# Optimization experiments

Measured on AMD Instinct MI355X. Metric: run time of the kernel, lower is better.

The kernel has to match this reference:

```python
import jax, jax.numpy as jnp
import numpy as np

B, S, D, H = 2, 2048, 1024, 16
DH = D // H


def setup_inputs() -> dict:
    key = jax.random.key(0)
    ks = jax.random.split(key, 7)
    scale = 1.0 / np.sqrt(D)
    queries = jax.random.normal(ks[0], (B, S, D), dtype=jnp.float32)
    keys_ = jax.random.normal(ks[1], (B, S, D), dtype=jnp.float32)
    values = jax.random.normal(ks[2], (B, S, D), dtype=jnp.float32)
    mask = jnp.tril(jnp.ones((S, S), dtype=jnp.int32))[None, None]  # causal [1,1,S,S]
    Wq = jax.random.normal(ks[3], (D, D), dtype=jnp.float32) * scale
    Wk = jax.random.normal(ks[4], (D, D), dtype=jnp.float32) * scale
    Wv = jax.random.normal(ks[5], (D, D), dtype=jnp.float32) * scale
    Wo = jax.random.normal(ks[6], (D, D), dtype=jnp.float32) * scale
    return {"queries": queries, "keys": keys_, "values": values, "mask": mask,
            "Wq": Wq, "Wk": Wk, "Wv": Wv, "Wo": Wo}


def reference(queries, keys, values, mask, Wq, Wk, Wv, Wo):
    # linear projections (nn.Linear, no bias): x @ W.T
    def split_heads(x, W):
        return (x @ W.T).reshape(B, -1, H, DH).transpose(0, 2, 1, 3)  # [B,H,S,DH]

    q = split_heads(queries, Wq)
    k = split_heads(keys, Wk)
    v = split_heads(values, Wv)

    scores = jnp.einsum('bhqd,bhkd->bhqk', q, k) / jnp.sqrt(jnp.float32(DH))
    scores = jnp.where(mask == 0, jnp.float32(-jnp.inf), scores)
    weights = jax.nn.softmax(scores, axis=-1)  # dropout p=0.0 -> identity
    out = jnp.einsum('bhqk,bhkd->bhqd', weights, v)
    out = out.transpose(0, 2, 1, 3).reshape(B, -1, D)
    return out @ Wo.T
```

## Files before the change

kernel.cpp:

```cpp
#include <hip/hip_runtime.h>
#include <hip/hip_bf16.h>


typedef unsigned short u16;
typedef __attribute__((ext_vector_type(8))) short bf16x8;
typedef __attribute__((ext_vector_type(4))) float f32x4;
typedef __attribute__((ext_vector_type(4))) short s16x4;

#define DEVI static __device__ __forceinline__
#define SCL 0.18033688011112042f
#define GLDS(g, l) __builtin_amdgcn_global_load_lds( \
    (const __attribute__((address_space(1))) unsigned*)(g), \
    (__attribute__((address_space(3))) unsigned*)(l), 16, 0, 0)

DEVI u16 f2bf(float f) {
  __hip_bfloat16 h = __float2bfloat16(f);
  union { __hip_bfloat16 h; u16 u; } c; c.h = h;
  return c.u;
}

DEVI bf16x8 cvt8(f32x4 a, f32x4 b) {
  bf16x8 r;
  r[0] = (short)f2bf(a[0]); r[1] = (short)f2bf(a[1]);
  r[2] = (short)f2bf(a[2]); r[3] = (short)f2bf(a[3]);
  r[4] = (short)f2bf(b[0]); r[5] = (short)f2bf(b[1]);
  r[6] = (short)f2bf(b[2]); r[7] = (short)f2bf(b[3]);
  return r;
}

template <int F32>
DEVI void load_pair(f32x4* lo, f32x4* hi, bf16x8* bb, const void* P,
                    size_t o0, size_t o1) {
  if constexpr (F32) {
    const float* p0 = (const float*)P + o0;
    const float* p1 = (const float*)P + o1;
    lo[0] = *(const f32x4*)p0; hi[0] = *(const f32x4*)(p0 + 4);
    lo[1] = *(const f32x4*)p1; hi[1] = *(const f32x4*)(p1 + 4);
  } else {
    bb[0] = *(const bf16x8*)((const u16*)P + o0);
    bb[1] = *(const bf16x8*)((const u16*)P + o1);
  }
}

template <int F32>
DEVI void finish_pair(f32x4* lo, f32x4* hi, bf16x8* bb, u16* dst, int e0, int e1) {
  if constexpr (F32) { bb[0] = cvt8(lo[0], hi[0]); bb[1] = cvt8(lo[1], hi[1]); }
  *(bf16x8*)(dst + e0) = bb[0];
  *(bf16x8*)(dst + e1) = bb[1];
}

template <int MODE, int O32>
DEVI void epilogue(f32x4 (&acc)[4][4], void* C, int tileM, int tileN,
                   int wr, int wc, int lr, int lg, float oscale) {
  constexpr int N = 1024;
  if constexpr (MODE == 0) {
#pragma unroll
    for (int m = 0; m < 4; ++m) {
      const int row0 = tileM + wr + m * 16 + lg * 4;
#pragma unroll
      for (int n = 0; n < 4; ++n) {
        const int col = tileN + wc + n * 16 + lr;
#pragma unroll
        for (int j = 0; j < 4; ++j) {
          if constexpr (O32)
            ((float*)C)[(size_t)(row0 + j) * N + col] = acc[m][n][j] * oscale;
          else
            ((u16*)C)[(size_t)(row0 + j) * N + col] = f2bf(acc[m][n][j] * oscale);
        }
      }
    }
  } else if constexpr (MODE == 1) {
    u16* Cv = (u16*)C;
#pragma unroll
    for (int m = 0; m < 4; ++m) {
      const int row0 = tileM + wr + m * 16 + lg * 4;
      const int bb = row0 >> 11, s0 = row0 & 2047;
#pragma unroll
      for (int n = 0; n < 4; ++n) {
        const int col = tileN + wc + n * 16 + lr;
        s16x4 pk;
#pragma unroll
        for (int j = 0; j < 4; ++j) pk[j] = (short)f2bf(acc[m][n][j]);
        *(s16x4*)(Cv + ((size_t)(col + (bb << 10)) << 11) + s0) = pk;
      }
    }
  } else {
    u16* Cv = (u16*)C;
#pragma unroll
    for (int m = 0; m < 4; ++m) {
      const int row0 = tileM + wr + m * 16 + lg * 4;
      const int bb = row0 >> 11, s0 = row0 & 2047;
#pragma unroll
      for (int n = 0; n < 4; ++n) {
        const int col = tileN + wc + n * 16 + lr;
        const size_t base = ((size_t)((bb << 4) + (col >> 6)) * 2048 + s0) * 64 + (col & 63);
#pragma unroll
        for (int j = 0; j < 4; ++j)
          Cv[base + (size_t)j * 64] = f2bf(acc[m][n][j]);
      }
    }
  }
}

template <int A32, int W32, int MODE, int O32>
DEVI void gemm_core(u16* sA0, u16* sA1, u16* sB0, u16* sB1,
                    const void* A, const void* W, void* C,
                    int tileM, int tileN, float oscale) {
  constexpr int K = 1024;
  const int tid = threadIdx.x;
  const int lane = tid & 63;
  const int wave = tid >> 6;
  const int wr = (wave >> 1) * 64;
  const int wc = (wave & 1) * 64;
  const int lr = lane & 15, lg = lane >> 4;

  f32x4 acc[4][4] = {};

  const int e0 = tid * 8;
  const int e1 = 2048 + tid * 8;
  const int r0 = e0 >> 5, c0 = e0 & 31;
  const int r1 = e1 >> 5, c1 = e1 & 31;
  const size_t oA0 = (size_t)(tileM + r0) * K + c0;
  const size_t oA1 = (size_t)(tileM + r1) * K + c1;
  const size_t oB0 = (size_t)(tileN + r0) * K + c0;
  const size_t oB1 = (size_t)(tileN + r1) * K + c1;

  f32x4 alo[2], ahi[2], blo[2], bhi[2];
  bf16x8 ab[2], bb[2];

  load_pair<A32>(alo, ahi, ab, A, oA0, oA1);
  load_pair<W32>(blo, bhi, bb, W, oB0, oB1);
  finish_pair<A32>(alo, ahi, ab, sA0, e0, e1);
  finish_pair<W32>(blo, bhi, bb, sB0, e0, e1);
  __syncthreads();

  for (int k0 = 0; k0 < K; k0 += 32) {
    u16* cA = (k0 & 32) ? sA1 : sA0;
    u16* cB = (k0 & 32) ? sB1 : sB0;
    u16* nA = (k0 & 32) ? sA0 : sA1;
    u16* nB = (k0 & 32) ? sB0 : sB1;

    bf16x8 af[4], bfr[4];
#pragma unroll
    for (int m = 0; m < 4; ++m)
      af[m] = *(const bf16x8*)(cA + (wr + m * 16 + lr) * 32 + lg * 8);
#pragma unroll
    for (int n = 0; n < 4; ++n)
      bfr[n] = *(const bf16x8*)(cB + (wc + n * 16 + lr) * 32 + lg * 8);

    const bool more = (k0 + 32 < K);
    if (more) {
      load_pair<A32>(alo, ahi, ab, A, oA0 + k0 + 32, oA1 + k0 + 32);
      load_pair<W32>(blo, bhi, bb, W, oB0 + k0 + 32, oB1 + k0 + 32);
    }

#pragma unroll
    for (int m = 0; m < 4; ++m)
#pragma unroll
      for (int n = 0; n < 4; ++n)
        acc[m][n] = __builtin_amdgcn_mfma_f32_16x16x32_bf16(af[m], bfr[n], acc[m][n], 0, 0, 0);

    if (more) {
      finish_pair<A32>(alo, ahi, ab, nA, e0, e1);
      finish_pair<W32>(blo, bhi, bb, nB, e0, e1);
    }
    __syncthreads();
  }
  epilogue<MODE, O32>(acc, C, tileM, tileN, wr, wc, lr, lg, oscale);
}

DEVI void tile_remap(int& tileM, int& tileN) {
  const int i = blockIdx.x + 8 * blockIdx.y;
  const int c = i & 7, s = i >> 3;
  tileM = (c * 4 + (s & 3)) * 128;
  tileN = (s >> 2) * 128;
}

template <int IN32>
__global__ void __launch_bounds__(256, 3)
gemm_qkv(const void* __restrict__ q, const void* __restrict__ wq, u16* __restrict__ Qp,
         const void* __restrict__ k, const void* __restrict__ wk, u16* __restrict__ Kh,
         const void* __restrict__ v, const void* __restrict__ wv, u16* __restrict__ Vt) {
  __shared__ __align__(16) u16 sA[2][128 * 32];
  __shared__ __align__(16) u16 sB[2][128 * 32];
  int tileM, tileN;
  tile_remap(tileM, tileN);
  if (blockIdx.z == 0)
    gemm_core<IN32, IN32, 0, 0>(sA[0], sA[1], sB[0], sB[1], q, wq, Qp, tileM, tileN, SCL);
  else if (blockIdx.z == 1)
    gemm_core<IN32, IN32, 2, 0>(sA[0], sA[1], sB[0], sB[1], k, wk, Kh, tileM, tileN, 1.f);
  else
    gemm_core<IN32, IN32, 1, 0>(sA[0], sA[1], sB[0], sB[1], v, wv, Vt, tileM, tileN, 1.f);
}

template <int W32, int O32>
__global__ void __launch_bounds__(256, 3)
gemm_out(const u16* __restrict__ A, const void* __restrict__ W, void* __restrict__ C) {
  __shared__ __align__(16) u16 sA[2][128 * 32];
  __shared__ __align__(16) u16 sB[2][128 * 32];
  int tileM, tileN;
  tile_remap(tileM, tileN);
  gemm_core<0, W32, 0, O32>(sA[0], sA[1], sB[0], sB[1], A, W, C, tileM, tileN, 1.f);
}


DEVI void stage_klds(const u16* __restrict__ Kb, const u16* __restrict__ Vb,
                     u16* sKb, u16* sVb, int kt, int w, int lane) {
  const int kr = lane >> 3;
  const int kg = (lane & 7) ^ kr;
  const u16* gk = Kb + (size_t)(kt + w * 16 + kr) * 64 + kg * 8;
  const int vr = lane >> 2;
  const int vg = (lane & 3) ^ ((lane >> 3) & 3);
  const u16* gv = Vb + (size_t)(w * 32 + vr) * 2048 + kt + vg * 8;
  u16* dk = sKb + w * 1024;
  u16* dv = sVb + w * 1024;
  GLDS(gk, dk);
  GLDS(gk + 8 * 64, dk + 512);
  GLDS(gv, dv);
  GLDS(gv + (size_t)16 * 2048, dv + 512);
}

__global__ void __launch_bounds__(128, 3)
attn_kernel(const u16* Qp, const u16* __restrict__ Kh,
            const u16* __restrict__ Vt, u16* AO) {
  __shared__ __align__(16) u16 sK[3][2048];
  __shared__ __align__(16) u16 sV[3][2048];
  const int tid = threadIdx.x;
  const int lane = tid & 63;
  const int w = tid >> 6;
  const int lr = lane & 15;
  const int lg = lane >> 4;

  const int id = blockIdx.x;
  const int xcd = id & 7;
  const int slot = id >> 3;
  const int bh = xcd * 4 + (slot & 3);
  const int band = 63 - (slot >> 2);
  const int b = bh >> 4;
  const int h = bh & 15;
  const int r0 = band * 32;

  const u16* Kb = Kh + (size_t)bh * 2048 * 64;
  const u16* Vb = Vt + (size_t)bh * 64 * 2048;

  const int qrow = r0 + w * 16 + lr;
  const u16* Qw = Qp + ((size_t)(b * 2048 + qrow) << 10) + h * 64;
  const bf16x8 qf0 = *(const bf16x8*)(Qw + lg * 8);
  const bf16x8 qf1 = *(const bf16x8*)(Qw + 32 + lg * 8);

  f32x4 o[4] = {};
  float mr = -INFINITY, ls = 0.f;
  const int nt = band + 1;

  stage_klds(Kb, Vb, sK[0], sV[0], 0, w, lane);

#pragma unroll 1
  for (int t = 0; t < nt; ++t) {
    if (t + 1 < nt) {
      const int bi = (t + 1) % 3;
      stage_klds(Kb, Vb, sK[bi], sV[bi], (t + 1) * 32, w, lane);
      asm volatile("s_waitcnt vmcnt(4)" ::: "memory");
    } else {
      asm volatile("s_waitcnt vmcnt(0)" ::: "memory");
    }
    asm volatile("s_barrier" ::: "memory");
    __builtin_amdgcn_s_setprio(1);

    {
      const int bi = t % 3;
      const u16* sKb = sK[bi];
      const u16* sVb = sV[bi];
      const int sw = lr & 7;
      const bf16x8 kf0 = *(const bf16x8*)(sKb + lr * 64 + ((lg ^ sw) * 8));
      const bf16x8 kf1 = *(const bf16x8*)(sKb + lr * 64 + (((4 + lg) ^ sw) * 8));
      const bf16x8 kf2 = *(const bf16x8*)(sKb + (16 + lr) * 64 + ((lg ^ sw) * 8));
      const bf16x8 kf3 = *(const bf16x8*)(sKb + (16 + lr) * 64 + (((4 + lg) ^ sw) * 8));

      const f32x4 z = {};
      f32x4 s0 = __builtin_amdgcn_mfma_f32_16x16x32_bf16(kf0, qf0, z, 0, 0, 0);
      s0 = __builtin_amdgcn_mfma_f32_16x16x32_bf16(kf1, qf1, s0, 0, 0, 0);
      f32x4 s1 = __builtin_amdgcn_mfma_f32_16x16x32_bf16(kf2, qf0, z, 0, 0, 0);
      s1 = __builtin_amdgcn_mfma_f32_16x16x32_bf16(kf3, qf1, s1, 0, 0, 0);

      float p[8];
#pragma unroll
      for (int j = 0; j < 4; ++j) { p[j] = s0[j]; p[4 + j] = s1[j]; }
      if (t == nt - 1) {
        const int kt0 = t * 32;
#pragma unroll
        for (int j = 0; j < 4; ++j) {
          if (kt0 + lg * 4 + j > qrow)      p[j] = -INFINITY;
          if (kt0 + 16 + lg * 4 + j > qrow) p[4 + j] = -INFINITY;
        }
      }

      const float tm = fmaxf(fmaxf(fmaxf(p[0], p[1]), fmaxf(p[2], p[3])),
                             fmaxf(fmaxf(p[4], p[5]), fmaxf(p[6], p[7])));
      if (!__all(tm <= mr + 11.5f)) {
        float tr_ = fmaxf(tm, __shfl_xor(tm, 16));
        tr_ = fmaxf(tr_, __shfl_xor(tr_, 32));
        const float mn = fmaxf(mr, tr_);
        const float fac = exp2f(mr - mn);
        mr = mn;
        ls *= fac;
#pragma unroll
        for (int j = 0; j < 4; ++j) {
          const float fj = __shfl(fac, lg * 4 + j);
#pragma unroll
          for (int d = 0; d < 4; ++d) o[d][j] *= fj;
        }
      }

#pragma unroll
      for (int i = 0; i < 8; ++i) p[i] = exp2f(p[i] - mr);
      ls += ((p[0] + p[1]) + (p[2] + p[3])) + ((p[4] + p[5]) + (p[6] + p[7]));

      bf16x8 pa;
#pragma unroll
      for (int i = 0; i < 8; ++i) pa[i] = (short)f2bf(p[i]);

      const int s2 = (lr >> 1) & 3;
#pragma unroll
      for (int d = 0; d < 4; ++d) {
        const u16* vrow = sVb + (16 * d + lr) * 32;
        const s16x4 v0 = *(const s16x4*)(vrow + (((lg >> 1) ^ s2) * 8) + (lg & 1) * 4);
        const s16x4 v1 = *(const s16x4*)(vrow + ((((lg >> 1) + 2) ^ s2) * 8) + (lg & 1) * 4);
        bf16x8 vf;
        vf[0] = v0[0]; vf[1] = v0[1]; vf[2] = v0[2]; vf[3] = v0[3];
        vf[4] = v1[0]; vf[5] = v1[1]; vf[6] = v1[2]; vf[7] = v1[3];
        o[d] = __builtin_amdgcn_mfma_f32_16x16x32_bf16(pa, vf, o[d], 0, 0, 0);
      }
    }
    __builtin_amdgcn_s_setprio(0);
  }

  float lt = ls + __shfl_xor(ls, 16);
  lt += __shfl_xor(lt, 32);
  const size_t orow = (size_t)(b * 2048 + r0 + w * 16 + lg * 4);
#pragma unroll
  for (int j = 0; j < 4; ++j) {
    const float inv = 1.0f / __shfl(lt, lg * 4 + j);
#pragma unroll
    for (int d = 0; d < 4; ++d)
      AO[(orow + j) * 1024 + h * 64 + 16 * d + lr] = f2bf(o[d][j] * inv);
  }
}

static int bytes_per_elem(void* p, long long n, void* pnext) {
  if (pnext) {
    ptrdiff_t d = (char*)pnext - (char*)p;
    if (d == n * 2) return 2;
    if (d == n * 4) return 4;
  }
  size_t sz = 0;
  if (hipMemPtrGetInfo(p, &sz) == hipSuccess && sz >= (size_t)(n * 2)) {
    if (sz < (size_t)(n * 4)) return 2;
    if (sz <= (size_t)(n * 8)) return 4;
  }
  return 4;
}

extern "C" void kernel_launch(void* const* d_in, const int* in_sizes, int n_in,
                              void* d_out, int out_size, void* d_ws, size_t ws_size,
                              hipStream_t stream) {
  void* q  = d_in[0];
  void* k  = d_in[1];
  void* v  = d_in[2];
  void* wq = d_in[4];
  void* wk = d_in[5];
  void* wv = d_in[6];
  void* wo = d_in[7];

  const int in32 = bytes_per_elem(q, in_sizes[0], k) == 4;
  const int w32  = bytes_per_elem(wq, in_sizes[4], wk) == 4;
  const int o32  = bytes_per_elem(d_out, out_size, nullptr) == 4;

  const size_t SZ = (size_t)4096 * 1024;
  u16* Qp = (u16*)d_ws;
  u16* Kh = Qp + SZ;
  u16* Vt = (u16*)d_out;
  u16* AO = Qp;

  if (in32)
    gemm_qkv<1><<<dim3(8, 32, 3), 256, 0, stream>>>(q, wq, Qp, k, wk, Kh, v, wv, Vt);
  else
    gemm_qkv<0><<<dim3(8, 32, 3), 256, 0, stream>>>(q, wq, Qp, k, wk, Kh, v, wv, Vt);

  attn_kernel<<<dim3(2048), 128, 0, stream>>>(Qp, Kh, Vt, AO);

  if (w32) {
    if (o32) gemm_out<1, 1><<<dim3(8, 32), 256, 0, stream>>>(AO, wo, d_out);
    else     gemm_out<1, 0><<<dim3(8, 32), 256, 0, stream>>>(AO, wo, d_out);
  } else {
    if (o32) gemm_out<0, 1><<<dim3(8, 32), 256, 0, stream>>>(AO, wo, d_out);
    else     gemm_out<0, 0><<<dim3(8, 32), 256, 0, stream>>>(AO, wo, d_out);
  }
}
```

Baseline: 127.4 us.

## Pad GEMM LDS rows and deepen A-operand prefetch with unrolled double-buffer loop

Pads the GEMM shared-memory tiles from a 32 to a 40-element row stride to cut LDS bank conflicts on the MFMA fragment reads. It also restructures the K loop into a manually unrolled pair of stages with fixed buffers. The A operand is now prefetched two K-steps ahead while W stays one step ahead, so more global-load latency is hidden. The cost is more live registers, which could hurt occupancy at launch_bounds(256,3), and more LDS per block.

```diff
diff --git a/kernel.cpp b/kernel.cpp
--- a/kernel.cpp
+++ b/kernel.cpp
@@ -9,6 +9,7 @@
 
 #define DEVI static __device__ __forceinline__
 #define SCL 0.18033688011112042f
+#define LDSW 40
 #define GLDS(g, l) __builtin_amdgcn_global_load_lds( \
     (const __attribute__((address_space(1))) unsigned*)(g), \
     (__attribute__((address_space(3))) unsigned*)(l), 16, 0, 0)
@@ -43,10 +44,10 @@
 }
 
 template <int F32>
-DEVI void finish_pair(f32x4* lo, f32x4* hi, bf16x8* bb, u16* dst, int e0, int e1) {
+DEVI void finish_pair(f32x4* lo, f32x4* hi, bf16x8* bb, u16* dst, int le0, int le1) {
   if constexpr (F32) { bb[0] = cvt8(lo[0], hi[0]); bb[1] = cvt8(lo[1], hi[1]); }
-  *(bf16x8*)(dst + e0) = bb[0];
-  *(bf16x8*)(dst + e1) = bb[1];
+  *(bf16x8*)(dst + le0) = bb[0];
+  *(bf16x8*)(dst + le1) = bb[1];
 }
 
 template <int MODE, int O32>
@@ -120,51 +121,68 @@
   const int e1 = 2048 + tid * 8;
   const int r0 = e0 >> 5, c0 = e0 & 31;
   const int r1 = e1 >> 5, c1 = e1 & 31;
+  const int le0 = r0 * LDSW + c0;
+  const int le1 = r1 * LDSW + c1;
   const size_t oA0 = (size_t)(tileM + r0) * K + c0;
   const size_t oA1 = (size_t)(tileM + r1) * K + c1;
   const size_t oB0 = (size_t)(tileN + r0) * K + c0;
   const size_t oB1 = (size_t)(tileN + r1) * K + c1;
 
-  f32x4 alo[2], ahi[2], blo[2], bhi[2];
-  bf16x8 ab[2], bb[2];
-
-  load_pair<A32>(alo, ahi, ab, A, oA0, oA1);
-  load_pair<W32>(blo, bhi, bb, W, oB0, oB1);
-  finish_pair<A32>(alo, ahi, ab, sA0, e0, e1);
-  finish_pair<W32>(blo, bhi, bb, sB0, e0, e1);
+  f32x4 aeLo[2], aeHi[2], aoLo[2], aoHi[2], wLo[2], wHi[2];
+  bf16x8 aeB[2], aoB[2], wB[2];
+
+  load_pair<A32>(aeLo, aeHi, aeB, A, oA0, oA1);
+  load_pair<W32>(wLo, wHi, wB, W, oB0, oB1);
+  finish_pair<A32>(aeLo, aeHi, aeB, sA0, le0, le1);
+  finish_pair<W32>(wLo, wHi, wB, sB0, le0, le1);
+  load_pair<A32>(aoLo, aoHi, aoB, A, oA0 + 32, oA1 + 32);
   __syncthreads();
 
-  for (int k0 = 0; k0 < K; k0 += 32) {
-    u16* cA = (k0 & 32) ? sA1 : sA0;
-    u16* cB = (k0 & 32) ? sB1 : sB0;
-    u16* nA = (k0 & 32) ? sA0 : sA1;
-    u16* nB = (k0 & 32) ? sB0 : sB1;
-
-    bf16x8 af[4], bfr[4];
-#pragma unroll
-    for (int m = 0; m < 4; ++m)
-      af[m] = *(const bf16x8*)(cA + (wr + m * 16 + lr) * 32 + lg * 8);
-#pragma unroll
-    for (int n = 0; n < 4; ++n)
-      bfr[n] = *(const bf16x8*)(cB + (wc + n * 16 + lr) * 32 + lg * 8);
-
-    const bool more = (k0 + 32 < K);
-    if (more) {
-      load_pair<A32>(alo, ahi, ab, A, oA0 + k0 + 32, oA1 + k0 + 32);
-      load_pair<W32>(blo, bhi, bb, W, oB0 + k0 + 32, oB1 + k0 + 32);
-    }
-
-#pragma unroll
-    for (int m = 0; m < 4; ++m)
+#pragma unroll 1
+  for (int it = 0; it < 16; ++it) {
+    const int kE = it * 64;
+    {
+      bf16x8 af[4], bfr[4];
+#pragma unroll
+      for (int m = 0; m < 4; ++m)
+        af[m] = *(const bf16x8*)(sA0 + (wr + m * 16 + lr) * LDSW + lg * 8);
 #pragma unroll
       for (int n = 0; n < 4; ++n)
-        acc[m][n] = __builtin_amdgcn_mfma_f32_16x16x32_bf16(af[m], bfr[n], acc[m][n], 0, 0, 0);
-
-    if (more) {
-      finish_pair<A32>(alo, ahi, ab, nA, e0, e1);
-      finish_pair<W32>(blo, bhi, bb, nB, e0, e1);
-    }
-    __syncthreads();
+        bfr[n] = *(const bf16x8*)(sB0 + (wc + n * 16 + lr) * LDSW + lg * 8);
+      if (it < 15) load_pair<A32>(aeLo, aeHi, aeB, A, oA0 + kE + 64, oA1 + kE + 64);
+      load_pair<W32>(wLo, wHi, wB, W, oB0 + kE + 32, oB1 + kE + 32);
+#pragma unroll
+      for (int m = 0; m < 4; ++m)
+#pragma unroll
+        for (int n = 0; n < 4; ++n)
+          acc[m][n] = __builtin_amdgcn_mfma_f32_16x16x32_bf16(af[m], bfr[n], acc[m][n], 0, 0, 0);
+      finish_pair<A32>(aoLo, aoHi, aoB, sA1, le0, le1);
+      finish_pair<W32>(wLo, wHi, wB, sB1, le0, le1);
+      __syncthreads();
+    }
+    {
+      bf16x8 af[4], bfr[4];
+#pragma unroll
+      for (int m = 0; m < 4; ++m)
+        af[m] = *(const bf16x8*)(sA1 + (wr + m * 16 + lr) * LDSW + lg * 8);
+#pragma unroll
+      for (int n = 0; n < 4; ++n)
+        bfr[n] = *(const bf16x8*)(sB1 + (wc + n * 16 + lr) * LDSW + lg * 8);
+      if (it < 15) {
+        load_pair<A32>(aoLo, aoHi, aoB, A, oA0 + kE + 96, oA1 + kE + 96);
+        load_pair<W32>(wLo, wHi, wB, W, oB0 + kE + 64, oB1 + kE + 64);
+      }
+#pragma unroll
+      for (int m = 0; m < 4; ++m)
+#pragma unroll
+        for (int n = 0; n < 4; ++n)
+          acc[m][n] = __builtin_amdgcn_mfma_f32_16x16x32_bf16(af[m], bfr[n], acc[m][n], 0, 0, 0);
+      if (it < 15) {
+        finish_pair<A32>(aeLo, aeHi, aeB, sA0, le0, le1);
+        finish_pair<W32>(wLo, wHi, wB, sB0, le0, le1);
+      }
+      __syncthreads();
+    }
   }
   epilogue<MODE, O32>(acc, C, tileM, tileN, wr, wc, lr, lg, oscale);
 }
@@ -181,8 +199,8 @@
 gemm_qkv(const void* __restrict__ q, const void* __restrict__ wq, u16* __restrict__ Qp,
          const void* __restrict__ k, const void* __restrict__ wk, u16* __restrict__ Kh,
          const void* __restrict__ v, const void* __restrict__ wv, u16* __restrict__ Vt) {
-  __shared__ __align__(16) u16 sA[2][128 * 32];
-  __shared__ __align__(16) u16 sB[2][128 * 32];
+  __shared__ __align__(16) u16 sA[2][128 * LDSW];
+  __shared__ __align__(16) u16 sB[2][128 * LDSW];
   int tileM, tileN;
   tile_remap(tileM, tileN);
   if (blockIdx.z == 0)
@@ -196,8 +214,8 @@
 template <int W32, int O32>
 __global__ void __launch_bounds__(256, 3)
 gemm_out(const u16* __restrict__ A, const void* __restrict__ W, void* __restrict__ C) {
-  __shared__ __align__(16) u16 sA[2][128 * 32];
-  __shared__ __align__(16) u16 sB[2][128 * 32];
+  __shared__ __align__(16) u16 sA[2][128 * LDSW];
+  __shared__ __align__(16) u16 sB[2][128 * LDSW];
   int tileM, tileN;
   tile_remap(tileM, tileN);
   gemm_core<0, W32, 0, O32>(sA[0], sA[1], sB[0], sB[1], A, W, C, tileM, tileN, 1.f);
```

Result: slower. 130.9 us (+2.8%).
